# Optimization experiments

Hardware: AMD Instinct MI355X
Metric: run time of the kernel (lower is better)

The kernel has to match this reference:

```python
import jax, jax.numpy as jnp
import numpy as np

B, D = 128, 16384
EPS = 0.05
MAX_DEPTH = 5
D_MAX = 1000.0


def setup_inputs() -> dict:
    key = jax.random.key(0)
    k1, k2 = jax.random.split(key)
    theta = jax.random.normal(k1, (B, D), dtype=jnp.float32)
    prec = jax.random.uniform(k2, (D,), dtype=jnp.float32)
    return {"theta": theta, "prec": prec}


def _energy(theta, prec):
    # per-chain potential energy U(theta): [B]
    return 0.5 * jnp.einsum('bd,d,bd->b', theta, prec, theta)


def _grad_energy(theta, prec):
    # mirrors torch autograd.grad(energy.sum(), theta)
    return jax.grad(lambda th: _energy(th, prec).sum())(theta)


def _bdot(a, b):
    return jnp.einsum('bd,bd->b', a, b)


def _leapfrog(theta, r, prec, eps):
    gU = _grad_energy(theta, prec)
    r = r - 0.5 * eps * gU
    theta = theta + eps * r
    e = _energy(theta, prec)
    gU = _grad_energy(theta, prec)
    r = r - 0.5 * eps * gU
    return theta, r, e


def _buildtree(theta, r, u, eps_dir, j, key, prec):
    # returns (theta_near, r_near, theta_far, r_far, theta_prop, n, s)
    if j == 0:
        th, rp, e = _leapfrog(theta, r, prec, eps_dir)
        H = e + 0.5 * _bdot(rp, rp)
        n_p = (u <= jnp.exp(-H)).astype(jnp.int32)
        s_p = (jnp.log(u) - D_MAX < -H).astype(jnp.int32)
        return th, rp, th, rp, th, n_p, s_p
    k1, k2, k3 = jax.random.split(key, 3)
    th_n, r_n, th_f, r_f, th_p, n_p, s_p = _buildtree(theta, r, u, eps_dir, j - 1, k1, prec)
    _, _, th_f2, r_f2, th_pp, n_pp, s_pp = _buildtree(th_f, r_f, u, eps_dir, j - 1, k2, prec)
    # accept proposal from second subtree with prob n'' / (n' + n''), masked by s'
    denom = jnp.maximum(n_p + n_pp, 1).astype(jnp.float32)
    flag = (jax.random.uniform(k3, n_p.shape) < n_pp.astype(jnp.float32) / denom) & (s_p >= 1)
    th_p = jnp.where(flag[:, None], th_pp, th_p)
    # u-turn check; v*(far - near) == theta_plus - theta_minus
    v = jnp.sign(eps_dir)
    d = th_f2 - th_n
    s_new = (s_p * s_pp
             * ((v * _bdot(d, r_n)) >= 0.0).astype(jnp.int32)
             * ((v * _bdot(d, r_f2)) >= 0.0).astype(jnp.int32))
    n_new = n_p + jnp.where(s_p >= 1, n_pp, 0)
    return th_n, r_n, th_f2, r_f2, th_p, n_new, s_new


def _sample_trajectory(theta0, prec, key):
    kr, ku, key = jax.random.split(key, 3)
    r0 = jax.random.normal(kr, theta0.shape, theta0.dtype)
    H0 = _energy(theta0, prec) + 0.5 * _bdot(r0, r0)
    u = jax.random.uniform(ku, H0.shape, theta0.dtype) * jnp.exp(-H0)
    theta_r = theta0
    theta_f = theta0
    r_r = r0
    r_f = r0
    theta_m = theta0
    n = jnp.ones((theta0.shape[0],), jnp.int32)
    s = jnp.ones((theta0.shape[0],), jnp.int32)
    for j in range(MAX_DEPTH):  # tree doubling, bounded depth (jit-friendly)
        key, kv, kt, ka = jax.random.split(key, 4)
        v = jnp.where(jax.random.normal(kv, ()) >= 0.0, 1.0, -1.0)
        neg = v < 0.0
        st_th = jnp.where(neg, theta_r, theta_f)
        st_r = jnp.where(neg, r_r, r_f)
        _, _, th_far, r_far, th_p, n_p, s_p = _buildtree(st_th, st_r, u, v * EPS, j, kt, prec)
        theta_r = jnp.where(neg, th_far, theta_r)
        r_r = jnp.where(neg, r_far, r_r)
        theta_f = jnp.where(neg, theta_f, th_far)
        r_f = jnp.where(neg, r_f, r_far)
        acc = jax.random.uniform(ka, n.shape) < jnp.minimum(
            n_p.astype(jnp.float32) / n.astype(jnp.float32), 1.0)
        acc = acc & (s >= 1) & (s_p >= 1)
        theta_m = jnp.where(acc[:, None], th_p, theta_m)
        n = n + jnp.where(s >= 1, n_p, 0)
        d = theta_f - theta_r
        s = (s * s_p
             * (_bdot(d, r_r) >= 0.0).astype(jnp.int32)
             * (_bdot(d, r_f) >= 0.0).astype(jnp.int32))
    return theta_m


def reference(theta, prec):
    return _sample_trajectory(theta, prec, jax.random.key(42))
```

## Files before the change

### kernel.cpp

```cpp
#include <hip/hip_runtime.h>
#include <cstdint>
#include <cstring>


#define PARTITIONABLE 1

constexpr int NCHAIN = 128;
constexpr int NDIM   = 16384;
constexpr int TPB    = 256;
constexpr int WGPC   = NDIM / (TPB * 4);
constexpr int NW     = NDIM / (64 * 4);
constexpr int NSLOT  = 62;
constexpr int NNODE  = 26;
constexpr float EPS  = 0.05f;

__host__ __device__ static inline void tf2(uint32_t k0, uint32_t k1,
                                           uint32_t x0, uint32_t x1,
                                           uint32_t& o0, uint32_t& o1) {
  const uint32_t ks2 = k0 ^ k1 ^ 0x1BD11BDAu;
  x0 += k0; x1 += k1;
#define TF_R(r) { x0 += x1; x1 = (x1 << (r)) | (x1 >> (32 - (r))); x1 ^= x0; }
  TF_R(13) TF_R(15) TF_R(26) TF_R(6)
  x0 += k1;  x1 += ks2 + 1u;
  TF_R(17) TF_R(29) TF_R(16) TF_R(24)
  x0 += ks2; x1 += k0 + 2u;
  TF_R(13) TF_R(15) TF_R(26) TF_R(6)
  x0 += k0;  x1 += k1 + 3u;
  TF_R(17) TF_R(29) TF_R(16) TF_R(24)
  x0 += k1;  x1 += ks2 + 4u;
  TF_R(13) TF_R(15) TF_R(26) TF_R(6)
  x0 += ks2; x1 += k0 + 5u;
#undef TF_R
  o0 = x0; o1 = x1;
}

__device__ static inline float u01(uint32_t bits) {
  return __uint_as_float((bits >> 9) | 0x3f800000u) - 1.0f;
}

__device__ static inline float erfinv32(float x) {
  float w = -log1pf(-x * x);
  float p;
  if (w < 5.0f) {
    w -= 2.5f;
    p = 2.81022636e-08f;
    p = fmaf(p, w, 3.43273939e-07f);
    p = fmaf(p, w, -3.5233877e-06f);
    p = fmaf(p, w, -4.39150654e-06f);
    p = fmaf(p, w, 0.00021858087f);
    p = fmaf(p, w, -0.00125372503f);
    p = fmaf(p, w, -0.00417768164f);
    p = fmaf(p, w, 0.246640727f);
    p = fmaf(p, w, 1.50140941f);
  } else {
    w = sqrtf(w) - 3.0f;
    p = -0.000200214257f;
    p = fmaf(p, w, 0.000100950558f);
    p = fmaf(p, w, 0.00134934322f);
    p = fmaf(p, w, -0.00367342844f);
    p = fmaf(p, w, 0.00573950773f);
    p = fmaf(p, w, -0.0076224613f);
    p = fmaf(p, w, 0.00943887047f);
    p = fmaf(p, w, 1.00167406f);
    p = fmaf(p, w, 2.83297682f);
  }
  return p * x;
}

__device__ static inline float norm_from_bits(uint32_t bits) {
  const float lo = __uint_as_float(0xBF7FFFFFu);
  float u = fmaxf(lo, fmaf(u01(bits), 2.0f, lo));
  return __uint_as_float(0x3FB504F3u) * erfinv32(u);
}

__device__ static inline float r0_elem(uint32_t k0, uint32_t k1, uint32_t i) {
#if PARTITIONABLE
  uint32_t a, c; tf2(k0, k1, 0u, i, a, c);
  return norm_from_bits(a ^ c);
#else
  const uint32_t H = (uint32_t)(NCHAIN * NDIM / 2);
  uint32_t a, c;
  if (i < H) { tf2(k0, k1, i, i + H, a, c); return norm_from_bits(a); }
  else       { tf2(k0, k1, i - H, i, a, c); return norm_from_bits(c); }
#endif
}

__device__ static inline float unif_chain(uint32_t k0, uint32_t k1, int b) {
#if PARTITIONABLE
  uint32_t a, c; tf2(k0, k1, 0u, (uint32_t)b, a, c);
  return u01(a ^ c);
#else
  uint32_t a, c;
  if (b < 64) { tf2(k0, k1, (uint32_t)b, (uint32_t)(b + 64), a, c); return u01(a); }
  else        { tf2(k0, k1, (uint32_t)(b - 64), (uint32_t)b, a, c); return u01(c); }
#endif
}

#define DPP_ADD(x, ctrl, rm)                                                   \
  (x) += __int_as_float(__builtin_amdgcn_update_dpp(                           \
      0, __float_as_int(x), (ctrl), (rm), 0xf, true));

__device__ static inline float wave_sum63(float x) {
  DPP_ADD(x, 0x111, 0xf)
  DPP_ADD(x, 0x112, 0xf)
  DPP_ADD(x, 0x114, 0xf)
  DPP_ADD(x, 0x118, 0xf)
  DPP_ADD(x, 0x142, 0xa)
  DPP_ADD(x, 0x143, 0xc)
  return x;
}

__device__ __forceinline__ float4 f4_pcfma(float he, const float4& pc,
                                           const float4& th, const float4& r) {
  return make_float4(fmaf(he, pc.x * th.x, r.x), fmaf(he, pc.y * th.y, r.y),
                     fmaf(he, pc.z * th.z, r.z), fmaf(he, pc.w * th.w, r.w));
}
__device__ __forceinline__ float4 f4_fma(float e, const float4& a, const float4& b) {
  return make_float4(fmaf(e, a.x, b.x), fmaf(e, a.y, b.y),
                     fmaf(e, a.z, b.z), fmaf(e, a.w, b.w));
}
__device__ __forceinline__ float f4_dotsub(const float4& a, const float4& b,
                                           const float4& r) {
  float d = (a.x - b.x) * r.x;
  d = fmaf(a.y - b.y, r.y, d);
  d = fmaf(a.z - b.z, r.z, d);
  d = fmaf(a.w - b.w, r.w, d);
  return d;
}

struct Params {
  uint32_t nk0[NNODE], nk1[NNODE];
  uint32_t ak0[5], ak1[5];
  int v[5];
};

struct Traj {
  float4 th, r, tho, ro, pc;
  float4 nt0, nt1, nt2, nt3, nt4;
  float4 nr0, nr1, nr2, nr3, nr4;
};
template <int L> __device__ __forceinline__ float4& NT(Traj& t) {
  if constexpr (L == 0) return t.nt0; else if constexpr (L == 1) return t.nt1;
  else if constexpr (L == 2) return t.nt2; else if constexpr (L == 3) return t.nt3;
  else return t.nt4;
}
template <int L> __device__ __forceinline__ float4& NR(Traj& t) {
  if constexpr (L == 0) return t.nr0; else if constexpr (L == 1) return t.nr1;
  else if constexpr (L == 2) return t.nr2; else if constexpr (L == 3) return t.nr3;
  else return t.nr4;
}

template <int P, int K, int M>
struct Merge {
  static __device__ __forceinline__ void run(Traj& t, float* __restrict__ partials,
                                             int chain, int wv, int lane, int& slot) {
    if constexpr (K < M) {
      const float4& nt = NT<P - 1 - K>(t);
      const float4& nr = NR<P - 1 - K>(t);
      float d1 = f4_dotsub(t.th, nt, nr);
      float d2 = f4_dotsub(t.th, nt, t.r);
      d1 = wave_sum63(d1);
      d2 = wave_sum63(d2);
      if (lane == 63) {
        partials[((size_t)(slot    ) * NCHAIN + chain) * NW + wv] = d1;
        partials[((size_t)(slot + 1) * NCHAIN + chain) * NW + wv] = d2;
      }
      slot += 2;
      Merge<P, K + 1, M>::run(t, partials, chain, wv, lane, slot);
    }
  }
};

template <int J, int I>
struct Leaf {
  static __device__ __forceinline__ void run(Traj& t, float e, float he,
                                             float* __restrict__ partials,
                                             int chain, int wv, int lane, int& slot) {
    t.r  = f4_pcfma(-he, t.pc, t.th, t.r);
    t.th = f4_fma(e, t.r, t.th);
    t.r  = f4_pcfma(-he, t.pc, t.th, t.r);
    constexpr int P = __builtin_popcount((unsigned)I);
    NT<P>(t) = t.th; NR<P>(t) = t.r;
    constexpr int M = __builtin_ctz(~(unsigned)I);
    Merge<P, 0, M>::run(t, partials, chain, wv, lane, slot);
    if constexpr (I + 1 < (1 << J))
      Leaf<J, I + 1>::run(t, e, he, partials, chain, wv, lane, slot);
  }
};

__launch_bounds__(TPB)
__global__ void k_traj0(const float* __restrict__ th0g, const float* __restrict__ precg,
                        uint32_t kr0, uint32_t kr1,
                        float* __restrict__ partials, Params P) {
  const int tid     = threadIdx.x;
  const int chain   = blockIdx.x / WGPC;
  const int sblk    = blockIdx.x % WGPC;
  const int dimBase = sblk * (TPB * 4) + tid * 4;
  const int lane    = tid & 63;
  const int wv      = sblk * (TPB / 64) + (tid >> 6);
  const uint32_t flat = (uint32_t)chain * NDIM + dimBase;

  Traj t;
  t.th = *reinterpret_cast<const float4*>(th0g + (size_t)chain * NDIM + dimBase);
  t.pc = *reinterpret_cast<const float4*>(precg + dimBase);
  t.r.x = r0_elem(kr0, kr1, flat + 0u);
  t.r.y = r0_elem(kr0, kr1, flat + 1u);
  t.r.z = r0_elem(kr0, kr1, flat + 2u);
  t.r.w = r0_elem(kr0, kr1, flat + 3u);
  t.tho = t.th; t.ro = t.r;

  int slot = 0;
  bool cur_fwd = true;

#define LEVEL(J)                                                               \
  {                                                                            \
    const bool fwd = P.v[J] > 0;                                               \
    if (fwd != cur_fwd) {                                                      \
      float4 tmp;                                                              \
      tmp = t.th; t.th = t.tho; t.tho = tmp;                                   \
      tmp = t.r;  t.r  = t.ro;  t.ro  = tmp;                                   \
    }                                                                          \
    cur_fwd = fwd;                                                             \
    const float e  = fwd ? EPS : -EPS;                                         \
    const float he = 0.5f * e;                                                 \
    Leaf<J, 0>::run(t, e, he, partials, chain, wv, lane, slot);                \
    float p1 = f4_dotsub(t.th, t.tho, t.r);                                    \
    float p2 = f4_dotsub(t.th, t.tho, t.ro);                                   \
    p1 = wave_sum63(p1);                                                       \
    p2 = wave_sum63(p2);                                                       \
    if (lane == 63) {                                                          \
      partials[((size_t)(slot    ) * NCHAIN + chain) * NW + wv] = p1;          \
      partials[((size_t)(slot + 1) * NCHAIN + chain) * NW + wv] = p2;          \
    }                                                                          \
    slot += 2;                                                                 \
  }

  LEVEL(0) LEVEL(1) LEVEL(2) LEVEL(3) LEVEL(4)
#undef LEVEL
}

struct SMs {
  int n0, s0, p0, n1, s1, p1, n2, s2, p2, n3, s3, p3, n4, s4, p4;
  int n, s, sel, slot, nodeidx, g;
};
template <int L> __device__ __forceinline__ int& SN(SMs& m) {
  if constexpr (L == 0) return m.n0; else if constexpr (L == 1) return m.n1;
  else if constexpr (L == 2) return m.n2; else if constexpr (L == 3) return m.n3;
  else return m.n4;
}
template <int L> __device__ __forceinline__ int& SS(SMs& m) {
  if constexpr (L == 0) return m.s0; else if constexpr (L == 1) return m.s1;
  else if constexpr (L == 2) return m.s2; else if constexpr (L == 3) return m.s3;
  else return m.s4;
}
template <int L> __device__ __forceinline__ int& SP(SMs& m) {
  if constexpr (L == 0) return m.p0; else if constexpr (L == 1) return m.p1;
  else if constexpr (L == 2) return m.p2; else if constexpr (L == 3) return m.p3;
  else return m.p4;
}

template <int P, int K, int M>
struct SMerge {
  static __device__ __forceinline__ void run(SMs& m, const float* dots_s,
                                             const float* unifs_s, float vj) {
    if constexpr (K < M) {
      constexpr int T = P - K;
      int n1 = SN<T-1>(m), s1 = SS<T-1>(m), p1 = SP<T-1>(m);
      int n2 = SN<T>(m),   s2 = SS<T>(m),   p2 = SP<T>(m);
      float d1 = dots_s[m.slot], d2 = dots_s[m.slot + 1];
      m.slot += 2;
      float uu = unifs_s[m.nodeidx]; m.nodeidx++;
      int dn = n1 + n2; if (dn < 1) dn = 1;
      bool fl = (uu < (float)n2 / (float)dn) && (s1 >= 1);
      SP<T-1>(m) = fl ? p2 : p1;
      SS<T-1>(m) = (s1 != 0 && s2 != 0 &&
                    (vj * d1 >= 0.0f) && (vj * d2 >= 0.0f)) ? 1 : 0;
      SN<T-1>(m) = n1 + ((s1 >= 1) ? n2 : 0);
      SMerge<P, K + 1, M>::run(m, dots_s, unifs_s, vj);
    }
  }
};

template <int J, int I>
struct SLeaf {
  static __device__ __forceinline__ void run(SMs& m, const float* dots_s,
                                             const float* unifs_s, float vj) {
    constexpr int P = __builtin_popcount((unsigned)I);
    SN<P>(m) = 1; SS<P>(m) = 1; SP<P>(m) = m.g; m.g++;
    constexpr int M = __builtin_ctz(~(unsigned)I);
    SMerge<P, 0, M>::run(m, dots_s, unifs_s, vj);
    if constexpr (I + 1 < (1 << J))
      SLeaf<J, I + 1>::run(m, dots_s, unifs_s, vj);
  }
};

template <int J>
__device__ __forceinline__ void sm_close(SMs& m, const float* dots_s,
                                         const float* unifs_s, int vj) {
  int n_p = SN<0>(m), s_p = SS<0>(m), th_p = SP<0>(m);
  float q1 = dots_s[m.slot], q2 = dots_s[m.slot + 1];
  m.slot += 2;
  float dm1, dm2;
  if (vj > 0) { dm1 = q2;  dm2 = q1; }
  else        { dm1 = -q1; dm2 = -q2; }
  float au = unifs_s[NNODE + J];
  float ratio = fminf((float)n_p / (float)m.n, 1.0f);
  bool acc = (au < ratio) && (m.s >= 1) && (s_p >= 1);
  if (acc) m.sel = th_p;
  m.n = m.n + ((m.s >= 1) ? n_p : 0);
  m.s = (m.s != 0 && s_p != 0 && (dm1 >= 0.0f) && (dm2 >= 0.0f)) ? 1 : 0;
}

__launch_bounds__(TPB)
__global__ void k_logic(const float* __restrict__ partials, int* __restrict__ selg,
                        Params P) {
  __shared__ float dots_s[NSLOT];
  __shared__ float unifs_s[NNODE + 5];
  const int chain = blockIdx.x;
  const int tid   = threadIdx.x;
  const int lane  = tid & 63;
  const int w     = tid >> 6;

  for (int s = w; s < NSLOT; s += TPB / 64) {
    float v = partials[((size_t)s * NCHAIN + chain) * NW + lane];
    v = wave_sum63(v);
    if (lane == 63) dots_s[s] = v;
  }
  if (tid < NNODE) unifs_s[tid] = unif_chain(P.nk0[tid], P.nk1[tid], chain);
  else if (tid < NNODE + 5)
    unifs_s[tid] = unif_chain(P.ak0[tid - NNODE], P.ak1[tid - NNODE], chain);
  __syncthreads();

  if (tid == 0) {
    SMs m;
    m.n = 1; m.s = 1; m.sel = -1; m.slot = 0; m.nodeidx = 0; m.g = 0;
#define SLEVEL(J)                                                              \
    {                                                                          \
      const float vj = (P.v[J] > 0) ? 1.0f : -1.0f;                            \
      SLeaf<J, 0>::run(m, dots_s, unifs_s, vj);                                \
      sm_close<J>(m, dots_s, unifs_s, P.v[J]);                                 \
    }
    SLEVEL(0) SLEVEL(1) SLEVEL(2) SLEVEL(3) SLEVEL(4)
#undef SLEVEL
    selg[chain] = m.sel;
  }
}

__launch_bounds__(TPB)
__global__ void k_gather(const float* __restrict__ th0g, const float* __restrict__ precg,
                         uint32_t kr0, uint32_t kr1,
                         const int* __restrict__ selg, float* __restrict__ outg,
                         Params P) {
  const int tid     = threadIdx.x;
  const int chain   = blockIdx.x / WGPC;
  const int sblk    = blockIdx.x % WGPC;
  const int dimBase = sblk * (TPB * 4) + tid * 4;
  const size_t off  = (size_t)chain * NDIM + dimBase;
  const uint32_t flat = (uint32_t)off;
  const int sel = selg[chain];

  float4 th = *reinterpret_cast<const float4*>(th0g + off);
  float4 outv = th;
  if (sel >= 0) {
    float4 pc = *reinterpret_cast<const float4*>(precg + dimBase);
    float4 r;
    r.x = r0_elem(kr0, kr1, flat + 0u);
    r.y = r0_elem(kr0, kr1, flat + 1u);
    r.z = r0_elem(kr0, kr1, flat + 2u);
    r.w = r0_elem(kr0, kr1, flat + 3u);
    float4 tho = th, ro = r;
    int g = 0;
    bool cur_fwd = true;
    bool fin = false;
    for (int j = 0; j < 5 && !fin; ++j) {
      const bool fwd = P.v[j] > 0;
      if (fwd != cur_fwd) {
        float4 tmp;
        tmp = th; th = tho; tho = tmp;
        tmp = r;  r  = ro;  ro  = tmp;
      }
      cur_fwd = fwd;
      const float e  = fwd ? EPS : -EPS;
      const float he = 0.5f * e;
      const int NL = 1 << j;
      for (int i = 0; i < NL; ++i) {
        r  = f4_pcfma(-he, pc, th, r);
        th = f4_fma(e, r, th);
        r  = f4_pcfma(-he, pc, th, r);
        if (g == sel) { outv = th; fin = true; break; }
        g++;
      }
    }
  }
  *reinterpret_cast<float4*>(outg + off) = outv;
}

static inline float host_bits_to_f(uint32_t fb) { float f; std::memcpy(&f, &fb, 4); return f; }

static void host_split(uint32_t k0, uint32_t k1, int nsub, uint32_t* o0, uint32_t* o1) {
#if PARTITIONABLE
  for (int i = 0; i < nsub; ++i) tf2(k0, k1, 0u, (uint32_t)i, o0[i], o1[i]);
#else
  uint32_t A[8], C[8], flat[16];
  for (int i = 0; i < nsub; ++i) tf2(k0, k1, (uint32_t)i, (uint32_t)(nsub + i), A[i], C[i]);
  for (int i = 0; i < nsub; ++i) { flat[i] = A[i]; flat[nsub + i] = C[i]; }
  for (int j = 0; j < nsub; ++j) { o0[j] = flat[2*j]; o1[j] = flat[2*j + 1]; }
#endif
}

static int host_vsign(uint32_t k0, uint32_t k1) {
  uint32_t a, c; tf2(k0, k1, 0u, 0u, a, c);
#if PARTITIONABLE
  uint32_t bits = a ^ c;
#else
  uint32_t bits = a;
#endif
  float f  = host_bits_to_f((bits >> 9) | 0x3f800000u) - 1.0f;
  float lo = host_bits_to_f(0xBF7FFFFFu);
  float u  = f * 2.0f + lo;
  return (u >= 0.0f) ? 1 : -1;
}

static void gen_nodes(uint32_t k0, uint32_t k1, int j,
                      uint32_t* nk0, uint32_t* nk1, int& idx) {
  if (j == 0) return;
  uint32_t o0[3], o1[3];
  host_split(k0, k1, 3, o0, o1);
  gen_nodes(o0[0], o1[0], j - 1, nk0, nk1, idx);
  gen_nodes(o0[1], o1[1], j - 1, nk0, nk1, idx);
  nk0[idx] = o0[2]; nk1[idx] = o1[2]; idx++;
}

extern "C" void kernel_launch(void* const* d_in, const int* in_sizes, int n_in,
                              void* d_out, int out_size, void* d_ws, size_t ws_size,
                              hipStream_t stream) {
  const float* th0  = (const float*)d_in[0];
  const float* prec = (const float*)d_in[1];
  float* out = (float*)d_out;

  float* partials = (float*)d_ws;
  int*   sel      = (int*)(partials + (size_t)NSLOT * NCHAIN * NW);

  uint32_t key0 = 0u, key1 = 42u;
  uint32_t s0[4], s1[4];
  host_split(key0, key1, 3, s0, s1);
  const uint32_t kr0 = s0[0], kr1 = s1[0];
  key0 = s0[2]; key1 = s1[2];

  Params P;
  int idx = 0;
  for (int j = 0; j < 5; ++j) {
    host_split(key0, key1, 4, s0, s1);
    key0 = s0[0]; key1 = s1[0];
    P.v[j] = host_vsign(s0[1], s1[1]);
    gen_nodes(s0[2], s1[2], j, P.nk0, P.nk1, idx);
    P.ak0[j] = s0[3]; P.ak1[j] = s1[3];
  }

  k_traj0<<<dim3(NCHAIN * WGPC), dim3(TPB), 0, stream>>>(
      th0, prec, kr0, kr1, partials, P);
  k_logic<<<dim3(NCHAIN), dim3(TPB), 0, stream>>>(partials, sel, P);
  k_gather<<<dim3(NCHAIN * WGPC), dim3(TPB), 0, stream>>>(
      th0, prec, kr0, kr1, sel, out, P);
}
```

Measured before the change: 116.3 us.

## Fuse logic kernel into gather, cache momentum, shorten wave reductions

Drops the separate per-chain logic kernel. Each gather workgroup now redundantly reduces the partial dot products and runs the NUTS tree state machine itself before replaying the trajectory. The initial momentum is saved to workspace in the first kernel so the gather kernel loads it instead of regenerating it with Threefry. Partial dot products are reduced only across 16-lane rows with DPP and stored four per wave, which removes the cross-row DPP steps but writes 4x more partials. Adds launch-bounds occupancy hints, extra global traffic for r0, and redundant serial logic in every workgroup (16 per chain).

```diff
diff --git a/kernel.cpp b/kernel.cpp
--- a/kernel.cpp
+++ b/kernel.cpp
@@ -9,7 +9,7 @@
 constexpr int NDIM   = 16384;
 constexpr int TPB    = 256;
 constexpr int WGPC   = NDIM / (TPB * 4);
-constexpr int NW     = NDIM / (64 * 4);
+constexpr int NP     = 256;
 constexpr int NSLOT  = 62;
 constexpr int NNODE  = 26;
 constexpr float EPS  = 0.05f;
@@ -109,6 +109,13 @@
   DPP_ADD(x, 0x143, 0xc)
   return x;
 }
+__device__ static inline float wave_sum15(float x) {
+  DPP_ADD(x, 0x111, 0xf)
+  DPP_ADD(x, 0x112, 0xf)
+  DPP_ADD(x, 0x114, 0xf)
+  DPP_ADD(x, 0x118, 0xf)
+  return x;
+}
 
 __device__ __forceinline__ float4 f4_pcfma(float he, const float4& pc,
                                            const float4& th, const float4& r) {
@@ -150,23 +157,28 @@
   else return t.nr4;
 }
 
+__device__ __forceinline__ void store_partial(float* __restrict__ partials,
+                                              int slot, int chain, int wv4,
+                                              int lane, float v) {
+  if ((lane & 15) == 15)
+    partials[((size_t)slot * NCHAIN + chain) * NP + wv4 + (lane >> 4)] = v;
+}
+
 template <int P, int K, int M>
 struct Merge {
   static __device__ __forceinline__ void run(Traj& t, float* __restrict__ partials,
-                                             int chain, int wv, int lane, int& slot) {
+                                             int chain, int wv4, int lane, int& slot) {
     if constexpr (K < M) {
       const float4& nt = NT<P - 1 - K>(t);
       const float4& nr = NR<P - 1 - K>(t);
       float d1 = f4_dotsub(t.th, nt, nr);
       float d2 = f4_dotsub(t.th, nt, t.r);
-      d1 = wave_sum63(d1);
-      d2 = wave_sum63(d2);
-      if (lane == 63) {
-        partials[((size_t)(slot    ) * NCHAIN + chain) * NW + wv] = d1;
-        partials[((size_t)(slot + 1) * NCHAIN + chain) * NW + wv] = d2;
-      }
+      d1 = wave_sum15(d1);
+      d2 = wave_sum15(d2);
+      store_partial(partials, slot,     chain, wv4, lane, d1);
+      store_partial(partials, slot + 1, chain, wv4, lane, d2);
       slot += 2;
-      Merge<P, K + 1, M>::run(t, partials, chain, wv, lane, slot);
+      Merge<P, K + 1, M>::run(t, partials, chain, wv4, lane, slot);
     }
   }
 };
@@ -175,29 +187,30 @@
 struct Leaf {
   static __device__ __forceinline__ void run(Traj& t, float e, float he,
                                              float* __restrict__ partials,
-                                             int chain, int wv, int lane, int& slot) {
+                                             int chain, int wv4, int lane, int& slot) {
     t.r  = f4_pcfma(-he, t.pc, t.th, t.r);
     t.th = f4_fma(e, t.r, t.th);
     t.r  = f4_pcfma(-he, t.pc, t.th, t.r);
     constexpr int P = __builtin_popcount((unsigned)I);
     NT<P>(t) = t.th; NR<P>(t) = t.r;
     constexpr int M = __builtin_ctz(~(unsigned)I);
-    Merge<P, 0, M>::run(t, partials, chain, wv, lane, slot);
+    Merge<P, 0, M>::run(t, partials, chain, wv4, lane, slot);
     if constexpr (I + 1 < (1 << J))
-      Leaf<J, I + 1>::run(t, e, he, partials, chain, wv, lane, slot);
-  }
-};
-
-__launch_bounds__(TPB)
+      Leaf<J, I + 1>::run(t, e, he, partials, chain, wv4, lane, slot);
+  }
+};
+
+__launch_bounds__(TPB, 4)
 __global__ void k_traj0(const float* __restrict__ th0g, const float* __restrict__ precg,
                         uint32_t kr0, uint32_t kr1,
-                        float* __restrict__ partials, Params P) {
+                        float* __restrict__ partials, float* __restrict__ r0save,
+                        Params P) {
   const int tid     = threadIdx.x;
   const int chain   = blockIdx.x / WGPC;
   const int sblk    = blockIdx.x % WGPC;
   const int dimBase = sblk * (TPB * 4) + tid * 4;
   const int lane    = tid & 63;
-  const int wv      = sblk * (TPB / 64) + (tid >> 6);
+  const int wv4     = (sblk * 4 + (tid >> 6)) * 4;
   const uint32_t flat = (uint32_t)chain * NDIM + dimBase;
 
   Traj t;
@@ -207,6 +220,7 @@
   t.r.y = r0_elem(kr0, kr1, flat + 1u);
   t.r.z = r0_elem(kr0, kr1, flat + 2u);
   t.r.w = r0_elem(kr0, kr1, flat + 3u);
+  *reinterpret_cast<float4*>(r0save + (size_t)flat) = t.r;
   t.tho = t.th; t.ro = t.r;
 
   int slot = 0;
@@ -223,15 +237,13 @@
     cur_fwd = fwd;                                                             \
     const float e  = fwd ? EPS : -EPS;                                         \
     const float he = 0.5f * e;                                                 \
-    Leaf<J, 0>::run(t, e, he, partials, chain, wv, lane, slot);                \
+    Leaf<J, 0>::run(t, e, he, partials, chain, wv4, lane, slot);               \
     float p1 = f4_dotsub(t.th, t.tho, t.r);                                    \
     float p2 = f4_dotsub(t.th, t.tho, t.ro);                                   \
-    p1 = wave_sum63(p1);                                                       \
-    p2 = wave_sum63(p2);                                                       \
-    if (lane == 63) {                                                          \
-      partials[((size_t)(slot    ) * NCHAIN + chain) * NW + wv] = p1;          \
-      partials[((size_t)(slot + 1) * NCHAIN + chain) * NW + wv] = p2;          \
-    }                                                                          \
+    p1 = wave_sum15(p1);                                                       \
+    p2 = wave_sum15(p2);                                                       \
+    store_partial(partials, slot,     chain, wv4, lane, p1);                   \
+    store_partial(partials, slot + 1, chain, wv4, lane, p2);                   \
     slot += 2;                                                                 \
   }
 
@@ -311,63 +323,50 @@
   m.s = (m.s != 0 && s_p != 0 && (dm1 >= 0.0f) && (dm2 >= 0.0f)) ? 1 : 0;
 }
 
-__launch_bounds__(TPB)
-__global__ void k_logic(const float* __restrict__ partials, int* __restrict__ selg,
-                        Params P) {
+__launch_bounds__(TPB, 4)
+__global__ void k_gather(const float* __restrict__ th0g, const float* __restrict__ precg,
+                         const float* __restrict__ partials, const float* __restrict__ r0save,
+                         float* __restrict__ outg, Params P) {
   __shared__ float dots_s[NSLOT];
   __shared__ float unifs_s[NNODE + 5];
-  const int chain = blockIdx.x;
-  const int tid   = threadIdx.x;
-  const int lane  = tid & 63;
-  const int w     = tid >> 6;
-
-  for (int s = w; s < NSLOT; s += TPB / 64) {
-    float v = partials[((size_t)s * NCHAIN + chain) * NW + lane];
-    v = wave_sum63(v);
-    if (lane == 63) dots_s[s] = v;
-  }
-  if (tid < NNODE) unifs_s[tid] = unif_chain(P.nk0[tid], P.nk1[tid], chain);
-  else if (tid < NNODE + 5)
-    unifs_s[tid] = unif_chain(P.ak0[tid - NNODE], P.ak1[tid - NNODE], chain);
-  __syncthreads();
-
-  if (tid == 0) {
-    SMs m;
-    m.n = 1; m.s = 1; m.sel = -1; m.slot = 0; m.nodeidx = 0; m.g = 0;
-#define SLEVEL(J)                                                              \
-    {                                                                          \
-      const float vj = (P.v[J] > 0) ? 1.0f : -1.0f;                            \
-      SLeaf<J, 0>::run(m, dots_s, unifs_s, vj);                                \
-      sm_close<J>(m, dots_s, unifs_s, P.v[J]);                                 \
-    }
-    SLEVEL(0) SLEVEL(1) SLEVEL(2) SLEVEL(3) SLEVEL(4)
-#undef SLEVEL
-    selg[chain] = m.sel;
-  }
-}
-
-__launch_bounds__(TPB)
-__global__ void k_gather(const float* __restrict__ th0g, const float* __restrict__ precg,
-                         uint32_t kr0, uint32_t kr1,
-                         const int* __restrict__ selg, float* __restrict__ outg,
-                         Params P) {
+
   const int tid     = threadIdx.x;
   const int chain   = blockIdx.x / WGPC;
   const int sblk    = blockIdx.x % WGPC;
   const int dimBase = sblk * (TPB * 4) + tid * 4;
   const size_t off  = (size_t)chain * NDIM + dimBase;
-  const uint32_t flat = (uint32_t)off;
-  const int sel = selg[chain];
+  const int lane    = tid & 63;
+  const int w       = tid >> 6;
+
+  for (int s = w; s < NSLOT; s += TPB / 64) {
+    const float4 v4 = *reinterpret_cast<const float4*>(
+        partials + ((size_t)s * NCHAIN + chain) * NP + lane * 4);
+    float v = (v4.x + v4.y) + (v4.z + v4.w);
+    v = wave_sum63(v);
+    if (lane == 63) dots_s[s] = v;
+  }
+  if (tid < NNODE) unifs_s[tid] = unif_chain(P.nk0[tid], P.nk1[tid], chain);
+  else if (tid < NNODE + 5)
+    unifs_s[tid] = unif_chain(P.ak0[tid - NNODE], P.ak1[tid - NNODE], chain);
+  __syncthreads();
+
+  SMs m;
+  m.n = 1; m.s = 1; m.sel = -1; m.slot = 0; m.nodeidx = 0; m.g = 0;
+#define SLEVEL(J)                                                              \
+  {                                                                            \
+    const float vj = (P.v[J] > 0) ? 1.0f : -1.0f;                              \
+    SLeaf<J, 0>::run(m, dots_s, unifs_s, vj);                                  \
+    sm_close<J>(m, dots_s, unifs_s, P.v[J]);                                   \
+  }
+  SLEVEL(0) SLEVEL(1) SLEVEL(2) SLEVEL(3) SLEVEL(4)
+#undef SLEVEL
+  const int sel = m.sel;
 
   float4 th = *reinterpret_cast<const float4*>(th0g + off);
   float4 outv = th;
   if (sel >= 0) {
     float4 pc = *reinterpret_cast<const float4*>(precg + dimBase);
-    float4 r;
-    r.x = r0_elem(kr0, kr1, flat + 0u);
-    r.y = r0_elem(kr0, kr1, flat + 1u);
-    r.z = r0_elem(kr0, kr1, flat + 2u);
-    r.w = r0_elem(kr0, kr1, flat + 3u);
+    float4 r  = *reinterpret_cast<const float4*>(r0save + off);
     float4 tho = th, ro = r;
     int g = 0;
     bool cur_fwd = true;
@@ -439,7 +438,7 @@
   float* out = (float*)d_out;
 
   float* partials = (float*)d_ws;
-  int*   sel      = (int*)(partials + (size_t)NSLOT * NCHAIN * NW);
+  float* r0save   = partials + (size_t)NSLOT * NCHAIN * NP;
 
   uint32_t key0 = 0u, key1 = 42u;
   uint32_t s0[4], s1[4];
@@ -458,8 +457,7 @@
   }
 
   k_traj0<<<dim3(NCHAIN * WGPC), dim3(TPB), 0, stream>>>(
-      th0, prec, kr0, kr1, partials, P);
-  k_logic<<<dim3(NCHAIN), dim3(TPB), 0, stream>>>(partials, sel, P);
+      th0, prec, kr0, kr1, partials, r0save, P);
   k_gather<<<dim3(NCHAIN * WGPC), dim3(TPB), 0, stream>>>(
-      th0, prec, kr0, kr1, sel, out, P);
-}
+      th0, prec, partials, r0save, out, P);
+}
```

Result: faster. 108.6 us (-6.6%).
